# Performance work log

Measured on AMD Instinct MI355X. Metric: run time of the kernel, lower is better.

Reference implementation:

```python
import jax, jax.numpy as jnp
import numpy as np

NUM_EXPERTS = 8
TOP_K = 2


def setup_inputs() -> dict:
    key = jax.random.key(0)
    ks = jax.random.split(key, 5)
    B, S, D, F, E = 4, 2048, 1024, 4096, NUM_EXPERTS
    scale = 0.02
    x = jax.random.normal(ks[0], (B, S, D), dtype=jnp.float32)
    W_gate = jax.random.normal(ks[1], (E, D), dtype=jnp.float32) * scale  # router: logits = x @ W_gate.T
    Wg = jax.random.normal(ks[2], (E, F, D), dtype=jnp.float32) * scale   # per-expert gate_proj
    Wu = jax.random.normal(ks[3], (E, F, D), dtype=jnp.float32) * scale   # per-expert up_proj
    Wd = jax.random.normal(ks[4], (E, D, F), dtype=jnp.float32) * scale   # per-expert down_proj
    return {"x": x, "W_gate": W_gate, "Wg": Wg, "Wu": Wu, "Wd": Wd}


def reference(x, W_gate, Wg, Wu, Wd):
    # Router: softmax over experts, then top-k, renormalize.
    gate_logits = jnp.einsum('bsd,ed->bse', x, W_gate)
    probs = jax.nn.softmax(gate_logits, axis=-1)
    top_w, top_i = jax.lax.top_k(probs, TOP_K)                # (B,S,K)
    top_w = top_w / jnp.sum(top_w, axis=-1, keepdims=True)

    output = jnp.zeros_like(x)
    for e in range(NUM_EXPERTS):
        # combined routing weight for expert e (0 for tokens not routed to e)
        w_e = jnp.sum(jnp.where(top_i == e, top_w, 0.0), axis=-1)  # (B,S)
        gate = jax.nn.silu(jnp.einsum('bsd,fd->bsf', x, Wg[e]))
        up = jnp.einsum('bsd,fd->bsf', x, Wu[e])
        out_e = jnp.einsum('bsf,df->bsd', gate * up, Wd[e])
        output = output + out_e * w_e[..., None]
    return output
```

## Files before the change

kernel.cpp:

```cpp
#include <hip/hip_runtime.h>
#include <hip/hip_bf16.h>

#define T_TOK 8192
#define D_DIM 1024
#define F_DIM 4096
#define NE 8

#define BM 128
#define BK 32

#define BM2 256
#define BN2 128
#define BK2 64
#define KT2 (D_DIM / BK2)

typedef _Float16 v8h __attribute__((ext_vector_type(8)));
typedef float f32x4 __attribute__((ext_vector_type(4)));

__device__ __forceinline__ void async_lds16(void* lds, const void* g) {
    __builtin_amdgcn_global_load_lds(
        (const __attribute__((address_space(1))) void*)g,
        (__attribute__((address_space(3))) void*)lds,
        16, 0, 0);
}

__global__ void router_kernel(const float* __restrict__ x,
                              const float* __restrict__ Wgate,
                              int* __restrict__ cnt,
                              int* __restrict__ rows,
                              float* __restrict__ wts) {
    int t = blockIdx.x;
    int lane = threadIdx.x;
    const float* xr = x + (size_t)t * D_DIM;
    float acc[NE];
#pragma unroll
    for (int e = 0; e < NE; ++e) acc[e] = 0.f;
#pragma unroll
    for (int i = 0; i < D_DIM / 64; ++i) {
        int d = i * 64 + lane;
        float xv = xr[d];
#pragma unroll
        for (int e = 0; e < NE; ++e) acc[e] += xv * Wgate[e * D_DIM + d];
    }
#pragma unroll
    for (int off = 32; off > 0; off >>= 1) {
#pragma unroll
        for (int e = 0; e < NE; ++e) acc[e] += __shfl_xor(acc[e], off, 64);
    }
    if (lane == 0) {
        int e0 = 0;
#pragma unroll
        for (int e = 1; e < NE; ++e) if (acc[e] > acc[e0]) e0 = e;
        int e1 = (e0 == 0) ? 1 : 0;
#pragma unroll
        for (int e = 0; e < NE; ++e) if (e != e0 && acc[e] > acc[e1]) e1 = e;
        float w0 = 1.f / (1.f + __expf(acc[e1] - acc[e0]));
        float w1 = 1.f - w0;
        int p0 = atomicAdd(&cnt[e0], 1);
        rows[e0 * T_TOK + p0] = 2 * t;
        wts[e0 * T_TOK + p0] = w0;
        int p1 = atomicAdd(&cnt[e1], 1);
        rows[e1 * T_TOK + p1] = 2 * t + 1;
        wts[e1 * T_TOK + p1] = w1;
    }
}

__global__ void f32to16_kernel(const float* __restrict__ src, _Float16* __restrict__ dst) {
    int i = blockIdx.x * blockDim.x + threadIdx.x;
    float4 v = ((const float4*)src)[i];
    union { _Float16 h[4]; uint2 u; } pk;
    pk.h[0] = (_Float16)v.x; pk.h[1] = (_Float16)v.y;
    pk.h[2] = (_Float16)v.z; pk.h[3] = (_Float16)v.w;
    *(uint2*)&dst[(size_t)i * 4] = pk.u;
}

__global__ __launch_bounds__(512, 2)
void gateup_kernel(const _Float16* __restrict__ Xh,
                   const _Float16* __restrict__ Wgh,
                   const _Float16* __restrict__ Wuh,
                   const int* __restrict__ cnt,
                   const int* __restrict__ rows,
                   const float* __restrict__ wts,
                   _Float16* __restrict__ H) {
    int e = blockIdx.z;
    int c = cnt[e];
    int row0 = blockIdx.y * BM2;
    if (row0 >= c) return;
    int col0 = blockIdx.x * BN2;

    __shared__ __align__(16) _Float16 Ab[2][BM2][BK2];
    __shared__ __align__(16) _Float16 Bb[2][BM2][BK2];
    __shared__ int hrow_s[BM2];
    __shared__ float w_s[BM2];

    int tid = threadIdx.x;
    int lane = tid & 63;
    int wv = tid >> 6;
    int wr = wv >> 2;
    int wc = wv & 3;

    if (tid < BM2) {
        int p = row0 + tid;
        if (p < c) { hrow_s[tid] = rows[e * T_TOK + p]; w_s[tid] = wts[e * T_TOK + p]; }
        else       { hrow_s[tid] = -1;                  w_s[tid] = 0.f; }
    }
    __syncthreads();

    int l8 = lane >> 3;
    int g  = lane & 7;
    int lg = g ^ l8;

    int r0 = wv * 16 + l8;
    int r1 = r0 + 8;

    int hA00 = hrow_s[r0],       hA01 = hrow_s[r1];
    int hA10 = hrow_s[128 + r0], hA11 = hrow_s[128 + r1];
    const _Float16* sA00 = Xh + (size_t)(hA00 >= 0 ? (hA00 >> 1) : 0) * D_DIM + lg * 8;
    const _Float16* sA01 = Xh + (size_t)(hA01 >= 0 ? (hA01 >> 1) : 0) * D_DIM + lg * 8;
    const _Float16* sA10 = Xh + (size_t)(hA10 >= 0 ? (hA10 >> 1) : 0) * D_DIM + lg * 8;
    const _Float16* sA11 = Xh + (size_t)(hA11 >= 0 ? (hA11 >> 1) : 0) * D_DIM + lg * 8;
    const _Float16* sB00 = Wgh + ((size_t)e * F_DIM + col0 + r0) * D_DIM + lg * 8;
    const _Float16* sB01 = Wgh + ((size_t)e * F_DIM + col0 + r1) * D_DIM + lg * 8;
    const _Float16* sB10 = Wuh + ((size_t)e * F_DIM + col0 + r0) * D_DIM + lg * 8;
    const _Float16* sB11 = Wuh + ((size_t)e * F_DIM + col0 + r1) * D_DIM + lg * 8;

    int stO0 = wv * 2048 + lane * 16;

    int m16 = lane & 15, q4 = lane >> 4;
    int rx = m16 & 7;
    int cb0 = ((q4 ^ rx) << 4);
    int cb1 = (((4 + q4) ^ rx) << 4);
    const char* arB = (const char*)Ab + (wr * 16 + m16) * 128;
    const char* brB = (const char*)Bb + m16 * 128 + wc * 4096;

    {
        char* a0 = (char*)Ab + stO0;
        char* b0 = (char*)Bb + stO0;
        async_lds16(b0,                sB00);
        async_lds16(b0 + 1024,         sB01);
        async_lds16(a0,                sA00);
        async_lds16(a0 + 1024,         sA01);
        async_lds16(b0 + 16384,        sB10);
        async_lds16(b0 + 16384 + 1024, sB11);
        async_lds16(a0 + 16384,        sA10);
        async_lds16(a0 + 16384 + 1024, sA11);
        asm volatile("s_waitcnt vmcnt(4)" ::: "memory");
        __builtin_amdgcn_s_barrier();
    }

    f32x4 accg[8][2], accu[8][2];
#pragma unroll
    for (int i = 0; i < 8; ++i)
#pragma unroll
        for (int j = 0; j < 2; ++j) { accg[i][j] = (f32x4)0.f; accu[i][j] = (f32x4)0.f; }

    int cur = 0;
#pragma unroll 1
    for (int t = 0; t < KT2; ++t) {
        int kn = (t + 1 < KT2) ? (t + 1) * BK2 : 0;
        int nb = cur ^ 1;
        const char* ar = arB + cur * 32768;
        const char* br = brB + cur * 32768;
        char* aD = (char*)Ab + nb * 32768 + stO0;
        char* bD = (char*)Bb + nb * 32768 + stO0;

        v8h af[4][2], bg[2][2], bu[2][2];

#pragma unroll
        for (int i = 0; i < 4; ++i) {
            af[i][0] = *(const v8h*)(ar + i * 4096 + cb0);
            af[i][1] = *(const v8h*)(ar + i * 4096 + cb1);
        }
#pragma unroll
        for (int j = 0; j < 2; ++j) {
            bg[j][0] = *(const v8h*)(br + j * 2048 + cb0);
            bg[j][1] = *(const v8h*)(br + j * 2048 + cb1);
        }
        async_lds16(bD,        sB00 + kn);
        async_lds16(bD + 1024, sB01 + kn);
        __builtin_amdgcn_s_barrier();
        __builtin_amdgcn_s_setprio(1);
#pragma unroll
        for (int i = 0; i < 4; ++i)
#pragma unroll
            for (int j = 0; j < 2; ++j) {
                accg[i][j] = __builtin_amdgcn_mfma_f32_16x16x32_f16(af[i][0], bg[j][0], accg[i][j], 0, 0, 0);
                accg[i][j] = __builtin_amdgcn_mfma_f32_16x16x32_f16(af[i][1], bg[j][1], accg[i][j], 0, 0, 0);
            }
        __builtin_amdgcn_s_setprio(0);
        asm volatile("s_waitcnt vmcnt(4)" ::: "memory");
        __builtin_amdgcn_s_barrier();

#pragma unroll
        for (int j = 0; j < 2; ++j) {
            bu[j][0] = *(const v8h*)(br + 16384 + j * 2048 + cb0);
            bu[j][1] = *(const v8h*)(br + 16384 + j * 2048 + cb1);
        }
        async_lds16(aD,        sA00 + kn);
        async_lds16(aD + 1024, sA01 + kn);
        __builtin_amdgcn_s_barrier();
        __builtin_amdgcn_s_setprio(1);
#pragma unroll
        for (int i = 0; i < 4; ++i)
#pragma unroll
            for (int j = 0; j < 2; ++j) {
                accu[i][j] = __builtin_amdgcn_mfma_f32_16x16x32_f16(af[i][0], bu[j][0], accu[i][j], 0, 0, 0);
                accu[i][j] = __builtin_amdgcn_mfma_f32_16x16x32_f16(af[i][1], bu[j][1], accu[i][j], 0, 0, 0);
            }
        __builtin_amdgcn_s_setprio(0);
        asm volatile("s_waitcnt vmcnt(4)" ::: "memory");
        __builtin_amdgcn_s_barrier();

#pragma unroll
        for (int i = 0; i < 4; ++i) {
            af[i][0] = *(const v8h*)(ar + (i + 4) * 4096 + cb0);
            af[i][1] = *(const v8h*)(ar + (i + 4) * 4096 + cb1);
        }
        async_lds16(bD + 16384,        sB10 + kn);
        async_lds16(bD + 16384 + 1024, sB11 + kn);
        __builtin_amdgcn_s_barrier();
        __builtin_amdgcn_s_setprio(1);
#pragma unroll
        for (int i = 0; i < 4; ++i)
#pragma unroll
            for (int j = 0; j < 2; ++j) {
                accg[i + 4][j] = __builtin_amdgcn_mfma_f32_16x16x32_f16(af[i][0], bg[j][0], accg[i + 4][j], 0, 0, 0);
                accg[i + 4][j] = __builtin_amdgcn_mfma_f32_16x16x32_f16(af[i][1], bg[j][1], accg[i + 4][j], 0, 0, 0);
            }
        __builtin_amdgcn_s_setprio(0);
        __builtin_amdgcn_s_barrier();

        async_lds16(aD + 16384,        sA10 + kn);
        async_lds16(aD + 16384 + 1024, sA11 + kn);
        __builtin_amdgcn_s_barrier();
        __builtin_amdgcn_s_setprio(1);
#pragma unroll
        for (int i = 0; i < 4; ++i)
#pragma unroll
            for (int j = 0; j < 2; ++j) {
                accu[i + 4][j] = __builtin_amdgcn_mfma_f32_16x16x32_f16(af[i][0], bu[j][0], accu[i + 4][j], 0, 0, 0);
                accu[i + 4][j] = __builtin_amdgcn_mfma_f32_16x16x32_f16(af[i][1], bu[j][1], accu[i + 4][j], 0, 0, 0);
            }
        __builtin_amdgcn_s_setprio(0);
        asm volatile("s_waitcnt vmcnt(4)" ::: "memory");
        __builtin_amdgcn_s_barrier();

        cur = nb;
    }

    int cl = lane & 15;
#pragma unroll
    for (int i = 0; i < 8; ++i) {
#pragma unroll
        for (int j = 0; j < 2; ++j) {
            f32x4 gv = accg[i][j];
            f32x4 uv = accu[i][j];
#pragma unroll
            for (int r4 = 0; r4 < 4; ++r4) {
                int r = i * 32 + wr * 16 + q4 * 4 + r4;
                int hr = hrow_s[r];
                if (hr < 0) continue;
                float gg = gv[r4];
                float h = gg / (1.f + __expf(-gg)) * w_s[r] * uv[r4];
                H[(size_t)hr * F_DIM + col0 + (wc * 2 + j) * 16 + cl] = (_Float16)h;
            }
        }
    }
}

__global__ __launch_bounds__(256, 2)
void down_kernel(const _Float16* __restrict__ H,
                 const _Float16* __restrict__ Wdh,
                 const int* __restrict__ cnt,
                 const int* __restrict__ rows,
                 float* __restrict__ O) {
    int e = blockIdx.z;
    int c = cnt[e];
    int row0 = blockIdx.y * BM;
    if (row0 >= c) return;
    int col0 = blockIdx.x * 128;

    __shared__ __align__(16) _Float16 As[BM][BK];
    __shared__ __align__(16) _Float16 Bs[128][BK];
    __shared__ int hrow_s[BM];

    int tid = threadIdx.x;
    int lane = tid & 63;
    int wave = tid >> 6;
    int wr = wave >> 1, wc = wave & 1;

    if (tid < BM) {
        int p = row0 + tid;
        hrow_s[tid] = (p < c) ? rows[e * T_TOK + p] : -1;
    }
    __syncthreads();

    int srow = tid >> 2;
    int kch = tid & 3;
    int hr0 = hrow_s[srow], hr1 = hrow_s[srow + 64];
    int r0 = (hr0 >= 0) ? hr0 : 0;
    int r1 = (hr1 >= 0) ? hr1 : 0;

    const _Float16* a0 = H + (size_t)r0 * F_DIM + kch * 8;
    const _Float16* a1 = H + (size_t)r1 * F_DIM + kch * 8;
    const _Float16* b0 = Wdh + ((size_t)e * D_DIM + col0 + srow) * F_DIM + kch * 8;
    const _Float16* b1 = b0 + (size_t)64 * F_DIM;

    _Float16* lA0 = &As[srow][kch * 8];
    _Float16* lA1 = &As[srow + 64][kch * 8];
    _Float16* lB0 = &Bs[srow][kch * 8];
    _Float16* lB1 = &Bs[srow + 64][kch * 8];

    f32x4 acc[4][4];
#pragma unroll
    for (int i = 0; i < 4; ++i)
#pragma unroll
        for (int j = 0; j < 4; ++j) acc[i][j] = (f32x4)0.f;

    int m16 = lane & 15, q8 = (lane >> 4) * 8;

    for (int k0 = 0; k0 < F_DIM; k0 += BK) {
        async_lds16(lA0, a0 + k0);
        async_lds16(lA1, a1 + k0);
        async_lds16(lB0, b0 + k0);
        async_lds16(lB1, b1 + k0);
        __syncthreads();

        v8h af[4], bf[4];
#pragma unroll
        for (int i = 0; i < 4; ++i)
            af[i] = *(const v8h*)&As[wr * 64 + i * 16 + m16][q8];
#pragma unroll
        for (int j = 0; j < 4; ++j)
            bf[j] = *(const v8h*)&Bs[wc * 64 + j * 16 + m16][q8];
#pragma unroll
        for (int i = 0; i < 4; ++i)
#pragma unroll
            for (int j = 0; j < 4; ++j)
                acc[i][j] = __builtin_amdgcn_mfma_f32_16x16x32_f16(af[i], bf[j], acc[i][j], 0, 0, 0);
        __syncthreads();
    }

    int q = lane >> 4, cl = lane & 15;
#pragma unroll
    for (int i = 0; i < 4; ++i) {
#pragma unroll
        for (int r4 = 0; r4 < 4; ++r4) {
            int r = wr * 64 + i * 16 + q * 4 + r4;
            int hr = hrow_s[r];
            if (hr < 0) continue;
#pragma unroll
            for (int j = 0; j < 4; ++j) {
                int col = col0 + wc * 64 + j * 16 + cl;
                O[(size_t)hr * D_DIM + col] = acc[i][j][r4];
            }
        }
    }
}

__global__ void combine_kernel(const float* __restrict__ O, float* __restrict__ out) {
    int t = blockIdx.x;
    int d = threadIdx.x;
    const float4* a = (const float4*)(O + (size_t)(2 * t) * D_DIM);
    const float4* b = (const float4*)(O + (size_t)(2 * t + 1) * D_DIM);
    float4 va = a[d], vb = b[d];
    float4 r; r.x = va.x + vb.x; r.y = va.y + vb.y; r.z = va.z + vb.z; r.w = va.w + vb.w;
    ((float4*)(out + (size_t)t * D_DIM))[d] = r;
}

extern "C" void kernel_launch(void* const* d_in, const int* in_sizes, int n_in,
                              void* d_out, int out_size, void* d_ws, size_t ws_size,
                              hipStream_t stream) {
    const float* x     = (const float*)d_in[0];
    const float* Wgate = (const float*)d_in[1];
    const float* Wg    = (const float*)d_in[2];
    const float* Wu    = (const float*)d_in[3];
    const float* Wd    = (const float*)d_in[4];
    float* out = (float*)d_out;

    char* w = (char*)d_ws;
    int*      cnt  = (int*)w;
    int*      rows = (int*)(w + 1024);
    float*    wts  = (float*)(w + 263168);
    _Float16* Xh   = (_Float16*)(w + 525312);

    const size_t OFF_WGH = 17302528;
    const size_t OFF_WUH = 84411392;
    const size_t OFF_WDH = 151520256;
    const size_t OFF_H   = 218629120;
    const size_t OFF_O   = 352846848;

    _Float16* Wgh = (_Float16*)(w + OFF_WGH);
    _Float16* Wuh = (_Float16*)(w + OFF_WUH);
    _Float16* Wdh = (_Float16*)(w + OFF_WDH);
    _Float16* H   = (_Float16*)(w + OFF_H);
    float*    O   = (float*)(w + OFF_O);

    hipMemsetAsync(w, 0, 1024, stream);

    router_kernel<<<T_TOK, 64, 0, stream>>>(x, Wgate, cnt, rows, wts);
    f32to16_kernel<<<(T_TOK * D_DIM / 4) / 256, 256, 0, stream>>>(x, Xh);

    const int WN4 = (NE * F_DIM * D_DIM / 4);
    f32to16_kernel<<<WN4 / 256, 256, 0, stream>>>(Wg, Wgh);
    f32to16_kernel<<<WN4 / 256, 256, 0, stream>>>(Wu, Wuh);
    f32to16_kernel<<<WN4 / 256, 256, 0, stream>>>(Wd, Wdh);

    gateup_kernel<<<dim3(F_DIM / BN2, T_TOK / BM2, NE), 512, 0, stream>>>(
        Xh, Wgh, Wuh, cnt, rows, wts, H);
    down_kernel<<<dim3(D_DIM / 128, T_TOK / BM, NE), 256, 0, stream>>>(
        H, Wdh, cnt, rows, O);
    combine_kernel<<<T_TOK, 256, 0, stream>>>(O, out);
}
```

Before: 1.289 ms.

## Collapse gate/up GEMM k-loop to one barrier per iteration with bulk prefetch

Restructures the gate/up GEMM main loop. It replaces the interleaved four-phase schedule (several s_barriers and partial vmcnt waits per k-step) with one vmcnt(0) plus one barrier at the top of each iteration. All eight async global-to-LDS prefetches for the next tile are then issued at once. LDS fragment reads now use inline-asm ds_read_b128 with immediate offsets, fenced by sched_barrier and lgkmcnt(0). The aim is to cut barrier and synchronisation overhead and address arithmetic, at the cost of less fine-grained overlap between loads and MFMA work.

Measured after the change: 1.183 ms. -8.2%, faster.

```diff
diff --git a/kernel.cpp b/kernel.cpp
--- a/kernel.cpp
+++ b/kernel.cpp
@@ -23,6 +23,17 @@
         (__attribute__((address_space(3))) void*)lds,
         16, 0, 0);
 }
+
+template<int OFF>
+__device__ __forceinline__ v8h ds128(unsigned a) {
+    v8h r;
+    asm volatile("ds_read_b128 %0, %1 offset:%2" : "=v"(r) : "v"(a), "n"(OFF));
+    return r;
+}
+
+#define LGKM0 asm volatile("s_waitcnt lgkmcnt(0)" ::: "memory")
+#define VMCNT0 asm volatile("s_waitcnt vmcnt(0)" ::: "memory")
+#define SB0 __builtin_amdgcn_sched_barrier(0)
 
 __global__ void router_kernel(const float* __restrict__ x,
                               const float* __restrict__ Wgate,
@@ -130,8 +141,13 @@
     int rx = m16 & 7;
     int cb0 = ((q4 ^ rx) << 4);
     int cb1 = (((4 + q4) ^ rx) << 4);
-    const char* arB = (const char*)Ab + (wr * 16 + m16) * 128;
-    const char* brB = (const char*)Bb + m16 * 128 + wc * 4096;
+
+    unsigned Abase = (unsigned)(size_t)(__attribute__((address_space(3))) void*)&Ab[0][0][0]
+                     + (unsigned)((wr * 16 + m16) * 128);
+    unsigned Bbase = (unsigned)(size_t)(__attribute__((address_space(3))) void*)&Bb[0][0][0]
+                     + (unsigned)(m16 * 128 + wc * 4096);
+    unsigned A0 = Abase + cb0, A1 = Abase + cb1;
+    unsigned B0 = Bbase + cb0, B1 = Bbase + cb1;
 
     {
         char* a0 = (char*)Ab + stO0;
@@ -144,8 +160,6 @@
         async_lds16(b0 + 16384 + 1024, sB11);
         async_lds16(a0 + 16384,        sA10);
         async_lds16(a0 + 16384 + 1024, sA11);
-        asm volatile("s_waitcnt vmcnt(4)" ::: "memory");
-        __builtin_amdgcn_s_barrier();
     }
 
     f32x4 accg[8][2], accu[8][2];
@@ -159,26 +173,42 @@
     for (int t = 0; t < KT2; ++t) {
         int kn = (t + 1 < KT2) ? (t + 1) * BK2 : 0;
         int nb = cur ^ 1;
-        const char* ar = arB + cur * 32768;
-        const char* br = brB + cur * 32768;
-        char* aD = (char*)Ab + nb * 32768 + stO0;
-        char* bD = (char*)Bb + nb * 32768 + stO0;
+
+        VMCNT0;
+        __builtin_amdgcn_s_barrier();
+        SB0;
+
+        {
+            char* aD = (char*)Ab + nb * 32768 + stO0;
+            char* bD = (char*)Bb + nb * 32768 + stO0;
+            async_lds16(bD,                sB00 + kn);
+            async_lds16(bD + 1024,         sB01 + kn);
+            async_lds16(aD,                sA00 + kn);
+            async_lds16(aD + 1024,         sA01 + kn);
+            async_lds16(bD + 16384,        sB10 + kn);
+            async_lds16(bD + 16384 + 1024, sB11 + kn);
+            async_lds16(aD + 16384,        sA10 + kn);
+            async_lds16(aD + 16384 + 1024, sA11 + kn);
+        }
+        SB0;
+
+        unsigned cOff = (unsigned)(cur * 32768);
+        unsigned a0 = A0 + cOff, a1 = A1 + cOff;
+        unsigned b0 = B0 + cOff, b1 = B1 + cOff;
 
         v8h af[4][2], bg[2][2], bu[2][2];
 
-#pragma unroll
-        for (int i = 0; i < 4; ++i) {
-            af[i][0] = *(const v8h*)(ar + i * 4096 + cb0);
-            af[i][1] = *(const v8h*)(ar + i * 4096 + cb1);
-        }
-#pragma unroll
-        for (int j = 0; j < 2; ++j) {
-            bg[j][0] = *(const v8h*)(br + j * 2048 + cb0);
-            bg[j][1] = *(const v8h*)(br + j * 2048 + cb1);
-        }
-        async_lds16(bD,        sB00 + kn);
-        async_lds16(bD + 1024, sB01 + kn);
-        __builtin_amdgcn_s_barrier();
+        af[0][0] = ds128<0>(a0);      af[0][1] = ds128<0>(a1);
+        af[1][0] = ds128<4096>(a0);   af[1][1] = ds128<4096>(a1);
+        af[2][0] = ds128<8192>(a0);   af[2][1] = ds128<8192>(a1);
+        af[3][0] = ds128<12288>(a0);  af[3][1] = ds128<12288>(a1);
+        bg[0][0] = ds128<0>(b0);      bg[0][1] = ds128<0>(b1);
+        bg[1][0] = ds128<2048>(b0);   bg[1][1] = ds128<2048>(b1);
+        bu[0][0] = ds128<16384>(b0);  bu[0][1] = ds128<16384>(b1);
+        bu[1][0] = ds128<18432>(b0);  bu[1][1] = ds128<18432>(b1);
+        LGKM0;
+        SB0;
+
         __builtin_amdgcn_s_setprio(1);
 #pragma unroll
         for (int i = 0; i < 4; ++i)
@@ -187,19 +217,6 @@
                 accg[i][j] = __builtin_amdgcn_mfma_f32_16x16x32_f16(af[i][0], bg[j][0], accg[i][j], 0, 0, 0);
                 accg[i][j] = __builtin_amdgcn_mfma_f32_16x16x32_f16(af[i][1], bg[j][1], accg[i][j], 0, 0, 0);
             }
-        __builtin_amdgcn_s_setprio(0);
-        asm volatile("s_waitcnt vmcnt(4)" ::: "memory");
-        __builtin_amdgcn_s_barrier();
-
-#pragma unroll
-        for (int j = 0; j < 2; ++j) {
-            bu[j][0] = *(const v8h*)(br + 16384 + j * 2048 + cb0);
-            bu[j][1] = *(const v8h*)(br + 16384 + j * 2048 + cb1);
-        }
-        async_lds16(aD,        sA00 + kn);
-        async_lds16(aD + 1024, sA01 + kn);
-        __builtin_amdgcn_s_barrier();
-        __builtin_amdgcn_s_setprio(1);
 #pragma unroll
         for (int i = 0; i < 4; ++i)
 #pragma unroll
@@ -208,17 +225,15 @@
                 accu[i][j] = __builtin_amdgcn_mfma_f32_16x16x32_f16(af[i][1], bu[j][1], accu[i][j], 0, 0, 0);
             }
         __builtin_amdgcn_s_setprio(0);
-        asm volatile("s_waitcnt vmcnt(4)" ::: "memory");
-        __builtin_amdgcn_s_barrier();
-
-#pragma unroll
-        for (int i = 0; i < 4; ++i) {
-            af[i][0] = *(const v8h*)(ar + (i + 4) * 4096 + cb0);
-            af[i][1] = *(const v8h*)(ar + (i + 4) * 4096 + cb1);
-        }
-        async_lds16(bD + 16384,        sB10 + kn);
-        async_lds16(bD + 16384 + 1024, sB11 + kn);
-        __builtin_amdgcn_s_barrier();
+        SB0;
+
+        af[0][0] = ds128<16384>(a0);  af[0][1] = ds128<16384>(a1);
+        af[1][0] = ds128<20480>(a0);  af[1][1] = ds128<20480>(a1);
+        af[2][0] = ds128<24576>(a0);  af[2][1] = ds128<24576>(a1);
+        af[3][0] = ds128<28672>(a0);  af[3][1] = ds128<28672>(a1);
+        LGKM0;
+        SB0;
+
         __builtin_amdgcn_s_setprio(1);
 #pragma unroll
         for (int i = 0; i < 4; ++i)
@@ -227,13 +242,6 @@
                 accg[i + 4][j] = __builtin_amdgcn_mfma_f32_16x16x32_f16(af[i][0], bg[j][0], accg[i + 4][j], 0, 0, 0);
                 accg[i + 4][j] = __builtin_amdgcn_mfma_f32_16x16x32_f16(af[i][1], bg[j][1], accg[i + 4][j], 0, 0, 0);
             }
-        __builtin_amdgcn_s_setprio(0);
-        __builtin_amdgcn_s_barrier();
-
-        async_lds16(aD + 16384,        sA10 + kn);
-        async_lds16(aD + 16384 + 1024, sA11 + kn);
-        __builtin_amdgcn_s_barrier();
-        __builtin_amdgcn_s_setprio(1);
 #pragma unroll
         for (int i = 0; i < 4; ++i)
 #pragma unroll
@@ -242,8 +250,6 @@
                 accu[i + 4][j] = __builtin_amdgcn_mfma_f32_16x16x32_f16(af[i][1], bu[j][1], accu[i + 4][j], 0, 0, 0);
             }
         __builtin_amdgcn_s_setprio(0);
-        asm volatile("s_waitcnt vmcnt(4)" ::: "memory");
-        __builtin_amdgcn_s_barrier();
 
         cur = nb;
     }
```
